# Optimization experiments

Hardware: AMD Instinct MI355X
Metric: run time of the kernel (lower is better)

The kernel has to match this reference:

```python
import jax, jax.numpy as jnp
import numpy as np

B = 500_000      # batch rows
F = 100          # fixed by x.view(-1, 100)
NT = 10          # number of tails (clusters)
C = 10           # cluster size (features per tail)
H = 7            # hidden = ceil(0.75 * C)


def setup_inputs() -> dict:
    key = jax.random.key(0)
    ks = jax.random.split(key, 7)
    x = jax.random.normal(ks[0], (B, F), dtype=jnp.float32)
    Wt = jax.random.normal(ks[1], (NT, H, C), dtype=jnp.float32) * 0.1
    hbias_t = jax.random.normal(ks[2], (NT, H), dtype=jnp.float32) * 0.1
    vbias_t = jax.random.normal(ks[3], (NT, C), dtype=jnp.float32) * 0.1
    Wh = jax.random.normal(ks[4], (H, NT), dtype=jnp.float32) * 0.1
    hbias_h = jax.random.normal(ks[5], (H,), dtype=jnp.float32) * 0.1
    vbias_h = jax.random.normal(ks[6], (NT,), dtype=jnp.float32) * 0.1
    clusters = jnp.arange(F, dtype=jnp.int32).reshape(NT, C)
    return {"x": x, "Wt": Wt, "hbias_t": hbias_t, "vbias_t": vbias_t,
            "Wh": Wh, "hbias_h": hbias_h, "vbias_h": vbias_h,
            "clusters": clusters}


def reference(x, Wt, hbias_t, vbias_t, Wh, hbias_h, vbias_h, clusters):
    x = x.reshape(-1, F)
    # fused gather: [B, NT, C]
    xc = x[:, clusters]
    # tail encoders: z = xc @ We.T + hbias  (We = Wt[t], shape [H, C])
    z = jnp.einsum('btc,thc->bth', xc, Wt) + hbias_t[None]          # [B, NT, H]
    # tail decoders (tied weights W.T): out = z @ We + vbias
    out = jnp.einsum('bth,thc->btc', z, Wt) + vbias_t[None]          # [B, NT, C]
    # per-sample, per-tail RMSE then log
    rmse = jnp.sqrt(jnp.mean((out - xc) ** 2, axis=-1))              # [B, NT]
    tails = jnp.log(rmse)                                            # [B, NT]
    # head autoencoder over tail scores
    zh = tails @ Wh.T + hbias_h                                      # [B, H]
    head_out = zh @ Wh + vbias_h                                     # [B, NT]
    return head_out, tails
```

## Files before the change

### kernel.cpp

```cpp
#include <hip/hip_runtime.h>


typedef float v2f __attribute__((ext_vector_type(2)));
typedef float v4f __attribute__((ext_vector_type(4)));

constexpr int F  = 100;
constexpr int NT = 10;
constexpr int C  = 10;
constexpr int H  = 7;
constexpr int BLOCK = 512;
constexpr int RPB   = 64;
constexpr int XSTR  = 102;

__device__ __forceinline__ int tail_col(int t) {
    return (t < 8) ? 10 * t : 10 * (t - 8) + 1;
}

__device__ __forceinline__ void do_tile(
    int t,
    float* __restrict__ xrow,
    const float* __restrict__ Wt,
    const float* __restrict__ hbt,
    const float* __restrict__ vbt)
{
    const int cb = t * 10;
    const v2f* __restrict__ xr2 = (const v2f*)(xrow + cb);
    v2f xc[5];
    #pragma unroll
    for (int c2 = 0; c2 < 5; ++c2) xc[c2] = xr2[c2];

    v2f out[5];
    #pragma unroll
    for (int c2 = 0; c2 < 5; ++c2) {
        out[c2].x = vbt[t * C + 2 * c2];
        out[c2].y = vbt[t * C + 2 * c2 + 1];
    }
    #pragma unroll
    for (int h = 0; h < H; ++h) {
        v2f w[5];
        #pragma unroll
        for (int c2 = 0; c2 < 5; ++c2) {
            w[c2].x = Wt[(t * H + h) * C + 2 * c2];
            w[c2].y = Wt[(t * H + h) * C + 2 * c2 + 1];
        }
        v2f za; za.x = hbt[t * H + h]; za.y = 0.f;
        #pragma unroll
        for (int c2 = 0; c2 < 5; ++c2)
            za = __builtin_elementwise_fma(xc[c2], w[c2], za);
        const float z = za.x + za.y;
        v2f zz; zz.x = z; zz.y = z;
        #pragma unroll
        for (int c2 = 0; c2 < 5; ++c2)
            out[c2] = __builtin_elementwise_fma(zz, w[c2], out[c2]);
    }
    v2f a2; a2.x = 0.f; a2.y = 0.f;
    #pragma unroll
    for (int c2 = 0; c2 < 5; ++c2) {
        const v2f d = out[c2] - xc[c2];
        a2 = __builtin_elementwise_fma(d, d, a2);
    }
    const float acc = a2.x + a2.y;
    xrow[tail_col(t)] = 0.5f * __logf(acc * 0.1f);
}

__global__ __launch_bounds__(BLOCK, 8) void kitnet_main(
    const float* __restrict__ x,
    const float* __restrict__ Wt,
    const float* __restrict__ hbt,
    const float* __restrict__ vbt,
    const float* __restrict__ Wh,
    const float* __restrict__ hbh,
    const float* __restrict__ vbh,
    float* __restrict__ head_out,
    float* __restrict__ tails_out,
    int B)
{
    __shared__ float xs[RPB * XSTR];

    const int tid = threadIdx.x;
    const long long r0 = (long long)blockIdx.x * RPB;
    const int nrows = (int)min((long long)RPB, (long long)B - r0);

    {
        const v4f* __restrict__ xg = (const v4f*)(x + r0 * F);
        const int n4 = nrows * (F / 4);
        #pragma unroll
        for (int k = 0; k < (RPB * F / 4 + BLOCK - 1) / BLOCK; ++k) {
            const int idx = tid + k * BLOCK;
            if (idx < n4) {
                v4f v = __builtin_nontemporal_load(&xg[idx]);
                const int row  = idx / 25;
                const int feat = (idx - row * 25) * 4;
                v2f* d = (v2f*)&xs[row * XSTR + feat];
                v2f lo; lo.x = v.x; lo.y = v.y;
                v2f hi; hi.x = v.z; hi.y = v.w;
                d[0] = lo; d[1] = hi;
            }
        }
    }
    __syncthreads();

    const int lane = tid & 63;
    const int wave = __builtin_amdgcn_readfirstlane(tid >> 6);
    float* xrow = &xs[lane * XSTR];

    do_tile(wave, xrow, Wt, hbt, vbt);
    if (wave < 2) do_tile(8 + wave, xrow, Wt, hbt, vbt);
    __syncthreads();

    const int ntask = nrows * 5;
    if (tid < ntask) {
        const int row = tid / 5;
        const int c0  = (tid - row * 5) * 2;
        const float* __restrict__ trow = &xs[row * XSTR];
        float tl[NT];
        #pragma unroll
        for (int t = 0; t < NT; ++t) tl[t] = trow[tail_col(t)];
        float zh[H];
        #pragma unroll
        for (int h = 0; h < H; ++h) {
            float s = hbh[h];
            #pragma unroll
            for (int t = 0; t < NT; ++t) s = fmaf(tl[t], Wh[h * NT + t], s);
            zh[h] = s;
        }
        float h0 = vbh[c0], h1 = vbh[c0 + 1];
        #pragma unroll
        for (int h = 0; h < H; ++h) {
            h0 = fmaf(zh[h], Wh[h * NT + c0],     h0);
            h1 = fmaf(zh[h], Wh[h * NT + c0 + 1], h1);
        }
        const long long o = (r0 + row) * NT + c0;
        v2f hv; hv.x = h0; hv.y = h1;
        v2f tv; tv.x = trow[tail_col(c0)]; tv.y = trow[tail_col(c0 + 1)];
        __builtin_nontemporal_store(hv, (v2f*)(head_out  + o));
        __builtin_nontemporal_store(tv, (v2f*)(tails_out + o));
    }
}

extern "C" void kernel_launch(void* const* d_in, const int* in_sizes, int n_in,
                              void* d_out, int out_size, void* d_ws, size_t ws_size,
                              hipStream_t stream) {
    const float* x   = (const float*)d_in[0];
    const float* Wt  = (const float*)d_in[1];
    const float* hbt = (const float*)d_in[2];
    const float* vbt = (const float*)d_in[3];
    const float* Wh  = (const float*)d_in[4];
    const float* hbh = (const float*)d_in[5];
    const float* vbh = (const float*)d_in[6];
    const int B = in_sizes[0] / F;
    float* head  = (float*)d_out;
    float* tails = head + (size_t)B * NT;
    const int grid = (B + RPB - 1) / RPB;
    kitnet_main<<<grid, BLOCK, 0, stream>>>(x, Wt, hbt, vbt, Wh, hbh, vbh,
                                            head, tails, B);
}
```

Before: 292.0 us.

## Process one row per thread directly from global memory, removing LDS staging

Replaces the shared-memory staged, wave-per-tail layout with a thread-per-row scheme. Each thread loads its 100 features with vector loads, computes all ten tail autoencoders and the head in registers, and writes its outputs. This removes the block barriers, the LDS traffic and the split of work across waves. In exchange, the global loads are strided per lane and no longer coalesced, and register pressure per thread rises.

```diff
diff --git a/kernel.cpp b/kernel.cpp
--- a/kernel.cpp
+++ b/kernel.cpp
@@ -8,62 +8,9 @@
 constexpr int NT = 10;
 constexpr int C  = 10;
 constexpr int H  = 7;
-constexpr int BLOCK = 512;
-constexpr int RPB   = 64;
-constexpr int XSTR  = 102;
+constexpr int BLOCK = 256;
 
-__device__ __forceinline__ int tail_col(int t) {
-    return (t < 8) ? 10 * t : 10 * (t - 8) + 1;
-}
-
-__device__ __forceinline__ void do_tile(
-    int t,
-    float* __restrict__ xrow,
-    const float* __restrict__ Wt,
-    const float* __restrict__ hbt,
-    const float* __restrict__ vbt)
-{
-    const int cb = t * 10;
-    const v2f* __restrict__ xr2 = (const v2f*)(xrow + cb);
-    v2f xc[5];
-    #pragma unroll
-    for (int c2 = 0; c2 < 5; ++c2) xc[c2] = xr2[c2];
-
-    v2f out[5];
-    #pragma unroll
-    for (int c2 = 0; c2 < 5; ++c2) {
-        out[c2].x = vbt[t * C + 2 * c2];
-        out[c2].y = vbt[t * C + 2 * c2 + 1];
-    }
-    #pragma unroll
-    for (int h = 0; h < H; ++h) {
-        v2f w[5];
-        #pragma unroll
-        for (int c2 = 0; c2 < 5; ++c2) {
-            w[c2].x = Wt[(t * H + h) * C + 2 * c2];
-            w[c2].y = Wt[(t * H + h) * C + 2 * c2 + 1];
-        }
-        v2f za; za.x = hbt[t * H + h]; za.y = 0.f;
-        #pragma unroll
-        for (int c2 = 0; c2 < 5; ++c2)
-            za = __builtin_elementwise_fma(xc[c2], w[c2], za);
-        const float z = za.x + za.y;
-        v2f zz; zz.x = z; zz.y = z;
-        #pragma unroll
-        for (int c2 = 0; c2 < 5; ++c2)
-            out[c2] = __builtin_elementwise_fma(zz, w[c2], out[c2]);
-    }
-    v2f a2; a2.x = 0.f; a2.y = 0.f;
-    #pragma unroll
-    for (int c2 = 0; c2 < 5; ++c2) {
-        const v2f d = out[c2] - xc[c2];
-        a2 = __builtin_elementwise_fma(d, d, a2);
-    }
-    const float acc = a2.x + a2.y;
-    xrow[tail_col(t)] = 0.5f * __logf(acc * 0.1f);
-}
-
-__global__ __launch_bounds__(BLOCK, 8) void kitnet_main(
+__global__ __launch_bounds__(BLOCK, 4) void kitnet_main(
     const float* __restrict__ x,
     const float* __restrict__ Wt,
     const float* __restrict__ hbt,
@@ -75,66 +22,93 @@
     float* __restrict__ tails_out,
     int B)
 {
-    __shared__ float xs[RPB * XSTR];
+    const long long row = (long long)blockIdx.x * BLOCK + threadIdx.x;
+    if (row >= B) return;
+    const float* __restrict__ xr = x + row * F;
 
-    const int tid = threadIdx.x;
-    const long long r0 = (long long)blockIdx.x * RPB;
-    const int nrows = (int)min((long long)RPB, (long long)B - r0);
+    float tl[NT];
 
-    {
-        const v4f* __restrict__ xg = (const v4f*)(x + r0 * F);
-        const int n4 = nrows * (F / 4);
+    #pragma unroll
+    for (int p = 0; p < 5; ++p) {
+        v4f q[5];
+        const v4f* __restrict__ qp = (const v4f*)(xr + 20 * p);
         #pragma unroll
-        for (int k = 0; k < (RPB * F / 4 + BLOCK - 1) / BLOCK; ++k) {
-            const int idx = tid + k * BLOCK;
-            if (idx < n4) {
-                v4f v = __builtin_nontemporal_load(&xg[idx]);
-                const int row  = idx / 25;
-                const int feat = (idx - row * 25) * 4;
-                v2f* d = (v2f*)&xs[row * XSTR + feat];
-                v2f lo; lo.x = v.x; lo.y = v.y;
-                v2f hi; hi.x = v.z; hi.y = v.w;
-                d[0] = lo; d[1] = hi;
+        for (int j = 0; j < 5; ++j) q[j] = qp[j];
+
+        #pragma unroll
+        for (int s = 0; s < 2; ++s) {
+            const int t = 2 * p + s;
+            v2f xc[5];
+            if (s == 0) {
+                xc[0].x = q[0].x; xc[0].y = q[0].y;
+                xc[1].x = q[0].z; xc[1].y = q[0].w;
+                xc[2].x = q[1].x; xc[2].y = q[1].y;
+                xc[3].x = q[1].z; xc[3].y = q[1].w;
+                xc[4].x = q[2].x; xc[4].y = q[2].y;
+            } else {
+                xc[0].x = q[2].z; xc[0].y = q[2].w;
+                xc[1].x = q[3].x; xc[1].y = q[3].y;
+                xc[2].x = q[3].z; xc[2].y = q[3].w;
+                xc[3].x = q[4].x; xc[3].y = q[4].y;
+                xc[4].x = q[4].z; xc[4].y = q[4].w;
             }
+
+            v2f out[5];
+            #pragma unroll
+            for (int c2 = 0; c2 < 5; ++c2) {
+                out[c2].x = vbt[t * C + 2 * c2];
+                out[c2].y = vbt[t * C + 2 * c2 + 1];
+            }
+            #pragma unroll
+            for (int h = 0; h < H; ++h) {
+                v2f w[5];
+                #pragma unroll
+                for (int c2 = 0; c2 < 5; ++c2) {
+                    w[c2].x = Wt[(t * H + h) * C + 2 * c2];
+                    w[c2].y = Wt[(t * H + h) * C + 2 * c2 + 1];
+                }
+                v2f za; za.x = hbt[t * H + h]; za.y = 0.f;
+                #pragma unroll
+                for (int c2 = 0; c2 < 5; ++c2)
+                    za = __builtin_elementwise_fma(xc[c2], w[c2], za);
+                const float z = za.x + za.y;
+                v2f zz; zz.x = z; zz.y = z;
+                #pragma unroll
+                for (int c2 = 0; c2 < 5; ++c2)
+                    out[c2] = __builtin_elementwise_fma(zz, w[c2], out[c2]);
+            }
+            v2f a2; a2.x = 0.f; a2.y = 0.f;
+            #pragma unroll
+            for (int c2 = 0; c2 < 5; ++c2) {
+                const v2f d = out[c2] - xc[c2];
+                a2 = __builtin_elementwise_fma(d, d, a2);
+            }
+            tl[t] = 0.5f * __logf((a2.x + a2.y) * 0.1f);
         }
     }
-    __syncthreads();
 
-    const int lane = tid & 63;
-    const int wave = __builtin_amdgcn_readfirstlane(tid >> 6);
-    float* xrow = &xs[lane * XSTR];
+    float zh[H];
+    #pragma unroll
+    for (int h = 0; h < H; ++h) {
+        float s = hbh[h];
+        #pragma unroll
+        for (int t = 0; t < NT; ++t) s = fmaf(tl[t], Wh[h * NT + t], s);
+        zh[h] = s;
+    }
 
-    do_tile(wave, xrow, Wt, hbt, vbt);
-    if (wave < 2) do_tile(8 + wave, xrow, Wt, hbt, vbt);
-    __syncthreads();
-
-    const int ntask = nrows * 5;
-    if (tid < ntask) {
-        const int row = tid / 5;
-        const int c0  = (tid - row * 5) * 2;
-        const float* __restrict__ trow = &xs[row * XSTR];
-        float tl[NT];
-        #pragma unroll
-        for (int t = 0; t < NT; ++t) tl[t] = trow[tail_col(t)];
-        float zh[H];
+    const long long o = row * NT;
+    #pragma unroll
+    for (int c2 = 0; c2 < 5; ++c2) {
+        float h0 = vbh[2 * c2], h1 = vbh[2 * c2 + 1];
         #pragma unroll
         for (int h = 0; h < H; ++h) {
-            float s = hbh[h];
-            #pragma unroll
-            for (int t = 0; t < NT; ++t) s = fmaf(tl[t], Wh[h * NT + t], s);
-            zh[h] = s;
+            h0 = fmaf(zh[h], Wh[h * NT + 2 * c2],     h0);
+            h1 = fmaf(zh[h], Wh[h * NT + 2 * c2 + 1], h1);
         }
-        float h0 = vbh[c0], h1 = vbh[c0 + 1];
-        #pragma unroll
-        for (int h = 0; h < H; ++h) {
-            h0 = fmaf(zh[h], Wh[h * NT + c0],     h0);
-            h1 = fmaf(zh[h], Wh[h * NT + c0 + 1], h1);
-        }
-        const long long o = (r0 + row) * NT + c0;
-        v2f hv; hv.x = h0; hv.y = h1;
-        v2f tv; tv.x = trow[tail_col(c0)]; tv.y = trow[tail_col(c0 + 1)];
-        __builtin_nontemporal_store(hv, (v2f*)(head_out  + o));
-        __builtin_nontemporal_store(tv, (v2f*)(tails_out + o));
+        v2f hv; hv.x = h0;         hv.y = h1;
+        v2f tv; tv.x = tl[2 * c2]; tv.y = tl[2 * c2 + 1];
+        __builtin_nontemporal_store(hv, (v2f*)(head_out  + o + 2 * c2));
+        __builtin_nontemporal_store(tv, (v2f*)(tails_out + o + 2 * c2));
     }
 }
 
@@ -151,7 +125,7 @@
     const int B = in_sizes[0] / F;
     float* head  = (float*)d_out;
     float* tails = head + (size_t)B * NT;
-    const int grid = (B + RPB - 1) / RPB;
+    const int grid = (B + BLOCK - 1) / BLOCK;
     kitnet_main<<<grid, BLOCK, 0, stream>>>(x, Wt, hbt, vbt, Wh, hbh, vbh,
                                             head, tails, B);
 }
```

Result: slower. 342.1 us (+17.2%).

## Double-buffer input tiles via async global-to-LDS loads in persistent blocks

Applied to the files above, without the earlier changes.

Converts the kernel into a persistent grid capped at 768 blocks that loops over 64-row chunks. The next chunk is prefetched into a second LDS buffer with global_load_lds, using hand-placed vmcnt waits and barriers so the load overlaps the current chunk's compute. It drops the padded row stride, remaps where the tail scores for tails 8 and 9 are stored, and reassigns the extra tiles to waves 6 and 7. The risks are LDS bank conflicts from the unpadded stride of 100, lower occupancy from the larger shared footprint, and fragile hand-written wait counts.

```diff
diff --git a/kernel.cpp b/kernel.cpp
--- a/kernel.cpp
+++ b/kernel.cpp
@@ -2,7 +2,6 @@
 
 
 typedef float v2f __attribute__((ext_vector_type(2)));
-typedef float v4f __attribute__((ext_vector_type(4)));
 
 constexpr int F  = 100;
 constexpr int NT = 10;
@@ -10,10 +9,25 @@
 constexpr int H  = 7;
 constexpr int BLOCK = 512;
 constexpr int RPB   = 64;
-constexpr int XSTR  = 102;
+constexpr int CHUNK_BYTES = RPB * F * 4;
+constexpr int NOPS = CHUNK_BYTES / 1024;
 
 __device__ __forceinline__ int tail_col(int t) {
-    return (t < 8) ? 10 * t : 10 * (t - 8) + 1;
+    return (t < 8) ? 10 * t : (t == 8 ? 61 : 71);
+}
+
+__device__ __forceinline__ void stage_issue(const float* __restrict__ x,
+                                            long long chunk, float* lds,
+                                            int wave, int lane, int tot_ops)
+{
+    const char* g0 = (const char*)x + chunk * (long long)CHUNK_BYTES + lane * 16;
+    char* l0 = (char*)lds;
+    for (int op = wave; op < tot_ops; op += 8) {
+        __builtin_amdgcn_global_load_lds(
+            (const __attribute__((address_space(1))) void*)(g0 + op * 1024),
+            (__attribute__((address_space(3))) void*)(l0 + op * 1024),
+            16, 0, 0);
+    }
 }
 
 __device__ __forceinline__ void do_tile(
@@ -63,7 +77,7 @@
     xrow[tail_col(t)] = 0.5f * __logf(acc * 0.1f);
 }
 
-__global__ __launch_bounds__(BLOCK, 8) void kitnet_main(
+__global__ __launch_bounds__(BLOCK, 6) void kitnet_main(
     const float* __restrict__ x,
     const float* __restrict__ Wt,
     const float* __restrict__ hbt,
@@ -75,66 +89,89 @@
     float* __restrict__ tails_out,
     int B)
 {
-    __shared__ float xs[RPB * XSTR];
+    __shared__ float xs[2][RPB * F];
 
-    const int tid = threadIdx.x;
-    const long long r0 = (long long)blockIdx.x * RPB;
-    const int nrows = (int)min((long long)RPB, (long long)B - r0);
+    const int tid  = threadIdx.x;
+    const int lane = tid & 63;
+    const int wave = __builtin_amdgcn_readfirstlane(tid >> 6);
+
+    const long long nchunks = ((long long)B + RPB - 1) / RPB;
+    long long chunk = blockIdx.x;
+    const int G = gridDim.x;
+    if (chunk >= nchunks) return;
 
     {
-        const v4f* __restrict__ xg = (const v4f*)(x + r0 * F);
-        const int n4 = nrows * (F / 4);
-        #pragma unroll
-        for (int k = 0; k < (RPB * F / 4 + BLOCK - 1) / BLOCK; ++k) {
-            const int idx = tid + k * BLOCK;
-            if (idx < n4) {
-                v4f v = __builtin_nontemporal_load(&xg[idx]);
-                const int row  = idx / 25;
-                const int feat = (idx - row * 25) * 4;
-                v2f* d = (v2f*)&xs[row * XSTR + feat];
-                v2f lo; lo.x = v.x; lo.y = v.y;
-                v2f hi; hi.x = v.z; hi.y = v.w;
-                d[0] = lo; d[1] = hi;
+        const long long rows0 = ((long long)B - chunk * RPB >= RPB)
+                                    ? RPB : ((long long)B - chunk * RPB);
+        const int tot0 = (int)((rows0 * F * 4 + 1023) / 1024);
+        stage_issue(x, chunk, xs[0], wave, lane, tot0);
+    }
+
+    int cur = 0;
+    for (; chunk < nchunks; chunk += G, cur ^= 1) {
+        const long long nxt = chunk + G;
+        const bool has_next  = (nxt < nchunks);
+        const bool next_full = has_next && (nxt * RPB + RPB <= (long long)B);
+
+        if (has_next) {
+            int tot = NOPS;
+            if (!next_full) {
+                const long long rows = (long long)B - nxt * RPB;
+                tot = (int)((rows * F * 4 + 1023) / 1024);
             }
+            stage_issue(x, nxt, xs[cur ^ 1], wave, lane, tot);
         }
-    }
-    __syncthreads();
 
-    const int lane = tid & 63;
-    const int wave = __builtin_amdgcn_readfirstlane(tid >> 6);
-    float* xrow = &xs[lane * XSTR];
+        if (next_full) {
+            if (wave == 0) asm volatile("s_waitcnt vmcnt(4)" ::: "memory");
+            else           asm volatile("s_waitcnt vmcnt(3)" ::: "memory");
+        } else {
+            asm volatile("s_waitcnt vmcnt(0)" ::: "memory");
+        }
+        asm volatile("s_barrier" ::: "memory");
 
-    do_tile(wave, xrow, Wt, hbt, vbt);
-    if (wave < 2) do_tile(8 + wave, xrow, Wt, hbt, vbt);
-    __syncthreads();
+        const long long rem = (long long)B - chunk * RPB;
+        const int nrows = (rem >= RPB) ? RPB : (int)rem;
+        float* xrow = &xs[cur][lane * F];
+        if (lane < nrows) {
+            do_tile(wave, xrow, Wt, hbt, vbt);
+            if (wave >= 6) do_tile(wave + 2, xrow, Wt, hbt, vbt);
+        }
 
-    const int ntask = nrows * 5;
-    if (tid < ntask) {
-        const int row = tid / 5;
-        const int c0  = (tid - row * 5) * 2;
-        const float* __restrict__ trow = &xs[row * XSTR];
-        float tl[NT];
-        #pragma unroll
-        for (int t = 0; t < NT; ++t) tl[t] = trow[tail_col(t)];
-        float zh[H];
-        #pragma unroll
-        for (int h = 0; h < H; ++h) {
-            float s = hbh[h];
+        asm volatile("s_waitcnt lgkmcnt(0)" ::: "memory");
+        __builtin_amdgcn_sched_barrier(0);
+        asm volatile("s_barrier" ::: "memory");
+
+        const int ntask = nrows * 5;
+        if (tid < ntask) {
+            const int row = tid / 5;
+            const int c0  = (tid - row * 5) * 2;
+            const float* __restrict__ trow = &xs[cur][row * F];
+            float tl[NT];
             #pragma unroll
-            for (int t = 0; t < NT; ++t) s = fmaf(tl[t], Wh[h * NT + t], s);
-            zh[h] = s;
+            for (int t = 0; t < NT; ++t) tl[t] = trow[tail_col(t)];
+            float zh[H];
+            #pragma unroll
+            for (int h = 0; h < H; ++h) {
+                float s = hbh[h];
+                #pragma unroll
+                for (int t = 0; t < NT; ++t) s = fmaf(tl[t], Wh[h * NT + t], s);
+                zh[h] = s;
+            }
+            float h0 = vbh[c0], h1 = vbh[c0 + 1];
+            #pragma unroll
+            for (int h = 0; h < H; ++h) {
+                h0 = fmaf(zh[h], Wh[h * NT + c0],     h0);
+                h1 = fmaf(zh[h], Wh[h * NT + c0 + 1], h1);
+            }
+            const long long o = (chunk * RPB + row) * NT + c0;
+            v2f hv; hv.x = h0; hv.y = h1;
+            v2f tv; tv.x = trow[tail_col(c0)]; tv.y = trow[tail_col(c0 + 1)];
+            *(v2f*)(head_out  + o) = hv;
+            *(v2f*)(tails_out + o) = tv;
         }
-        float h0 = vbh[c0], h1 = vbh[c0 + 1];
-        #pragma unroll
-        for (int h = 0; h < H; ++h) {
-            h0 = fmaf(zh[h], Wh[h * NT + c0],     h0);
-            h1 = fmaf(zh[h], Wh[h * NT + c0 + 1], h1);
-        }
-        const long long o = (r0 + row) * NT + c0;
-        v2f hv; hv.x = h0; hv.y = h1;
-        v2f tv; tv.x = trow[tail_col(c0)]; tv.y = trow[tail_col(c0 + 1)];
-        __builtin_nontemporal_store(hv, (v2f*)(head_out  + o));
-        __builtin_nontemporal_store(tv, (v2f*)(tails_out + o));
+
+        asm volatile("s_barrier" ::: "memory");
     }
 }
 
@@ -151,7 +188,8 @@
     const int B = in_sizes[0] / F;
     float* head  = (float*)d_out;
     float* tails = head + (size_t)B * NT;
-    const int grid = (B + RPB - 1) / RPB;
+    const long long nchunks = ((long long)B + RPB - 1) / RPB;
+    const int grid = (int)((nchunks < 768) ? nchunks : 768);
     kitnet_main<<<grid, BLOCK, 0, stream>>>(x, Wt, hbt, vbt, Wh, hbh, vbh,
                                             head, tails, B);
 }
```

After: 299.6 us. 1.03x slower.

## Stage input rows into LDS via direct global_load_lds and separate tail buffer

Applied to the files above, without the earlier changes.

The input tile is now copied straight from global memory into LDS with the global_load_lds builtin, one 1 KB contiguous chunk per wave op, which skips the register round trip and the repacking into a padded row stride. Because rows are now unpadded (stride 100), tail scores go into a separate small shared buffer instead of overwriting x slots. The two leftover tails are spread across all eight waves using 16 lanes each, and output stores become ordinary instead of nontemporal. The unpadded stride may raise LDS bank conflicts when the tail tiles read their rows, and the clamped address on the last block copies some redundant data.

```diff
diff --git a/kernel.cpp b/kernel.cpp
--- a/kernel.cpp
+++ b/kernel.cpp
@@ -2,7 +2,6 @@
 
 
 typedef float v2f __attribute__((ext_vector_type(2)));
-typedef float v4f __attribute__((ext_vector_type(4)));
 
 constexpr int F  = 100;
 constexpr int NT = 10;
@@ -10,21 +9,18 @@
 constexpr int H  = 7;
 constexpr int BLOCK = 512;
 constexpr int RPB   = 64;
-constexpr int XSTR  = 102;
-
-__device__ __forceinline__ int tail_col(int t) {
-    return (t < 8) ? 10 * t : 10 * (t - 8) + 1;
-}
+constexpr long long CHUNK_BYTES = (long long)RPB * F * 4;
+constexpr int TSTR = 12;
 
 __device__ __forceinline__ void do_tile(
     int t,
-    float* __restrict__ xrow,
+    const float* __restrict__ xrow,
+    float* __restrict__ tdst,
     const float* __restrict__ Wt,
     const float* __restrict__ hbt,
     const float* __restrict__ vbt)
 {
-    const int cb = t * 10;
-    const v2f* __restrict__ xr2 = (const v2f*)(xrow + cb);
+    const v2f* __restrict__ xr2 = (const v2f*)(xrow + t * 10);
     v2f xc[5];
     #pragma unroll
     for (int c2 = 0; c2 < 5; ++c2) xc[c2] = xr2[c2];
@@ -60,7 +56,7 @@
         a2 = __builtin_elementwise_fma(d, d, a2);
     }
     const float acc = a2.x + a2.y;
-    xrow[tail_col(t)] = 0.5f * __logf(acc * 0.1f);
+    tdst[t] = 0.5f * __logf(acc * 0.1f);
 }
 
 __global__ __launch_bounds__(BLOCK, 8) void kitnet_main(
@@ -75,47 +71,52 @@
     float* __restrict__ tails_out,
     int B)
 {
-    __shared__ float xs[RPB * XSTR];
+    __shared__ float xs[RPB * F];
+    __shared__ float ts[RPB * TSTR];
 
-    const int tid = threadIdx.x;
+    const int tid  = threadIdx.x;
+    const int lane = tid & 63;
+    const int wave = __builtin_amdgcn_readfirstlane(tid >> 6);
+
     const long long r0 = (long long)blockIdx.x * RPB;
     const int nrows = (int)min((long long)RPB, (long long)B - r0);
 
     {
-        const v4f* __restrict__ xg = (const v4f*)(x + r0 * F);
-        const int n4 = nrows * (F / 4);
-        #pragma unroll
-        for (int k = 0; k < (RPB * F / 4 + BLOCK - 1) / BLOCK; ++k) {
-            const int idx = tid + k * BLOCK;
-            if (idx < n4) {
-                v4f v = __builtin_nontemporal_load(&xg[idx]);
-                const int row  = idx / 25;
-                const int feat = (idx - row * 25) * 4;
-                v2f* d = (v2f*)&xs[row * XSTR + feat];
-                v2f lo; lo.x = v.x; lo.y = v.y;
-                v2f hi; hi.x = v.z; hi.y = v.w;
-                d[0] = lo; d[1] = hi;
-            }
+        const long long xbytes = (long long)B * F * 4;
+        const char* gbase = (const char*)x + r0 * F * 4 + lane * 16;
+        const char* gmax  = (const char*)x + xbytes - 16;
+        char* l0 = (char*)xs;
+        const int tot = (nrows == RPB) ? 25
+                                       : (int)(((long long)nrows * 400 + 1023) >> 10);
+        for (int op = wave; op < tot; op += 8) {
+            const char* ga = gbase + op * 1024;
+            if (ga > gmax) ga = gmax;
+            __builtin_amdgcn_global_load_lds(
+                (const __attribute__((address_space(1))) void*)ga,
+                (__attribute__((address_space(3))) void*)(l0 + op * 1024),
+                16, 0, 0);
         }
     }
     __syncthreads();
 
-    const int lane = tid & 63;
-    const int wave = __builtin_amdgcn_readfirstlane(tid >> 6);
-    float* xrow = &xs[lane * XSTR];
-
-    do_tile(wave, xrow, Wt, hbt, vbt);
-    if (wave < 2) do_tile(8 + wave, xrow, Wt, hbt, vbt);
+    if (lane < nrows)
+        do_tile(wave, &xs[lane * F], &ts[lane * TSTR], Wt, hbt, vbt);
+    if (lane < 16) {
+        const int t2   = 8 + (wave >> 2);
+        const int row2 = (wave & 3) * 16 + lane;
+        if (row2 < nrows)
+            do_tile(t2, &xs[row2 * F], &ts[row2 * TSTR], Wt, hbt, vbt);
+    }
     __syncthreads();
 
     const int ntask = nrows * 5;
     if (tid < ntask) {
         const int row = tid / 5;
         const int c0  = (tid - row * 5) * 2;
-        const float* __restrict__ trow = &xs[row * XSTR];
+        const float* __restrict__ trow = &ts[row * TSTR];
         float tl[NT];
         #pragma unroll
-        for (int t = 0; t < NT; ++t) tl[t] = trow[tail_col(t)];
+        for (int t = 0; t < NT; ++t) tl[t] = trow[t];
         float zh[H];
         #pragma unroll
         for (int h = 0; h < H; ++h) {
@@ -131,10 +132,10 @@
             h1 = fmaf(zh[h], Wh[h * NT + c0 + 1], h1);
         }
         const long long o = (r0 + row) * NT + c0;
-        v2f hv; hv.x = h0; hv.y = h1;
-        v2f tv; tv.x = trow[tail_col(c0)]; tv.y = trow[tail_col(c0 + 1)];
-        __builtin_nontemporal_store(hv, (v2f*)(head_out  + o));
-        __builtin_nontemporal_store(tv, (v2f*)(tails_out + o));
+        v2f hv; hv.x = h0;     hv.y = h1;
+        v2f tv; tv.x = tl[c0]; tv.y = tl[c0 + 1];
+        *(v2f*)(head_out  + o) = hv;
+        *(v2f*)(tails_out + o) = tv;
     }
 }
 
@@ -151,7 +152,7 @@
     const int B = in_sizes[0] / F;
     float* head  = (float*)d_out;
     float* tails = head + (size_t)B * NT;
-    const int grid = (B + RPB - 1) / RPB;
+    const int grid = (int)(((long long)B + RPB - 1) / RPB);
     kitnet_main<<<grid, BLOCK, 0, stream>>>(x, Wt, hbt, vbt, Wh, hbh, vbh,
                                             head, tails, B);
 }
```

After: 298.3 us. 1.02x slower.
